# Optimization experiments

Measured on AMD Instinct MI355X. Metric: run time of the kernel, lower is better.

Reference implementation:

```python
import jax, jax.numpy as jnp
import numpy as np

B, T, C_EMBD, C_ATT = 16, 1024, 2048, 2048


def wkv(time_decay, time_first, k, v):
    """Numerically-stable RWKV WKV recurrence (matches wkv_cuda).
    time_decay/time_first: [C]; k, v: [B, T, C] -> y: [B, T, C]."""
    w = -jnp.exp(time_decay)  # [C], decay is -exp(param)
    u = time_first
    Bn, Tn, Cn = k.shape

    def step(carry, kv_t):
        aa, bb, pp = carry          # each [B, C]
        kt, vt = kv_t               # [B, C]
        ww = u + kt
        p = jnp.maximum(pp, ww)
        e1 = jnp.exp(pp - p)
        e2 = jnp.exp(ww - p)
        y = (e1 * aa + e2 * vt) / (e1 * bb + e2)
        ww2 = pp + w
        p2 = jnp.maximum(ww2, kt)
        e1b = jnp.exp(ww2 - p2)
        e2b = jnp.exp(kt - p2)
        new = (e1b * aa + e2b * vt, e1b * bb + e2b, p2)
        return new, y

    init = (jnp.zeros((Bn, Cn), k.dtype),
            jnp.zeros((Bn, Cn), k.dtype),
            jnp.full((Bn, Cn), -1e38, k.dtype))
    kT = jnp.swapaxes(k, 0, 1)  # [T, B, C]
    vT = jnp.swapaxes(v, 0, 1)
    _, ys = jax.lax.scan(step, init, (kT, vT))
    return jnp.swapaxes(ys, 0, 1)  # [B, T, C]


def setup_inputs() -> dict:
    key = jax.random.key(0)
    ks = jax.random.split(key, 10)
    xav = np.sqrt(2.0 / (C_EMBD + C_ATT))
    inp = {
        "x": jax.random.normal(ks[0], (B, T, C_EMBD), jnp.float32),
        "time_decay": jax.random.normal(ks[1], (C_ATT,), jnp.float32) * 0.02,
        "time_first": jax.random.normal(ks[2], (C_ATT,), jnp.float32) * 0.02,
        "time_mix_k": jax.random.normal(ks[3], (1, 1, C_EMBD), jnp.float32) * 0.02,
        "time_mix_v": jax.random.normal(ks[4], (1, 1, C_EMBD), jnp.float32) * 0.02,
        "time_mix_r": jax.random.normal(ks[5], (1, 1, C_EMBD), jnp.float32) * 0.02,
        "key_w": jax.random.normal(ks[6], (C_ATT, C_EMBD), jnp.float32) * xav,
        "value_w": jax.random.normal(ks[7], (C_ATT, C_EMBD), jnp.float32) * xav,
        "receptance_w": jax.random.normal(ks[8], (C_ATT, C_EMBD), jnp.float32) * xav,
        "output_w": jax.random.normal(ks[9], (C_EMBD, C_ATT), jnp.float32) * xav,
    }
    return inp


def reference(x, time_decay, time_first, time_mix_k, time_mix_v, time_mix_r,
              key_w, value_w, receptance_w, output_w):
    # time shift: xx[:, t] = x[:, t-1], xx[:, 0] = 0
    xx = jnp.pad(x, ((0, 0), (1, 0), (0, 0)))[:, :-1]
    xk = x * time_mix_k + xx * (1 - time_mix_k)
    xv = x * time_mix_v + xx * (1 - time_mix_v)
    xr = x * time_mix_r + xx * (1 - time_mix_r)
    k = jnp.einsum('btc,dc->btd', xk, key_w)
    v = jnp.einsum('btc,dc->btd', xv, value_w)
    r = jnp.einsum('btc,dc->btd', xr, receptance_w)
    sr = jax.nn.sigmoid(r)
    rwkv = sr * wkv(time_decay, time_first, k, v)
    return jnp.einsum('btd,cd->btc', rwkv, output_w)
```

## Files before the change

kernel.cpp:

```cpp
#include <hip/hip_runtime.h>
#include <hip/hip_bf16.h>

#define BB 16
#define TT 1024
#define CC 2048
#define TS 32

typedef __attribute__((ext_vector_type(4))) float f32x4;
typedef __attribute__((ext_vector_type(8))) short bf16x8;

__device__ __forceinline__ unsigned short f2bf(float f) {
  union { float f; unsigned u; } x; x.f = f;
  unsigned r = x.u + 0x7fffu + ((x.u >> 16) & 1u);
  return (unsigned short)(r >> 16);
}
__device__ __forceinline__ float bf2f(unsigned short u) {
  union { unsigned u; float f; } x; x.u = ((unsigned)u) << 16;
  return x.f;
}

__device__ __forceinline__ ushort4 mix4(float4 a, float4 b, float4 m) {
  ushort4 o;
  o.x = f2bf(a.x * m.x + b.x * (1.f - m.x));
  o.y = f2bf(a.y * m.y + b.y * (1.f - m.y));
  o.z = f2bf(a.z * m.z + b.z * (1.f - m.z));
  o.w = f2bf(a.w * m.w + b.w * (1.f - m.w));
  return o;
}

__global__ void f2bf_all(const float* __restrict__ w0, const float* __restrict__ w1,
                         const float* __restrict__ w2, const float* __restrict__ w3,
                         unsigned short* __restrict__ o0, unsigned short* __restrict__ o1,
                         unsigned short* __restrict__ o2, unsigned short* __restrict__ o3,
                         int n4each) {
  const float* ws[4] = {w0, w1, w2, w3};
  unsigned short* os[4] = {o0, o1, o2, o3};
  int total = 4 * n4each;
  for (int i = blockIdx.x * blockDim.x + threadIdx.x; i < total;
       i += gridDim.x * blockDim.x) {
    int seg = i / n4each, j = i - seg * n4each;
    float4 v = ((const float4*)ws[seg])[j];
    ushort4 o;
    o.x = f2bf(v.x); o.y = f2bf(v.y); o.z = f2bf(v.z); o.w = f2bf(v.w);
    ((ushort4*)os[seg])[j] = o;
  }
}

__global__ void mix_kernel(const float* __restrict__ x,
                           const float* __restrict__ tmk,
                           const float* __restrict__ tmv,
                           const float* __restrict__ tmr,
                           unsigned short* __restrict__ xk,
                           unsigned short* __restrict__ xv,
                           unsigned short* __restrict__ xr,
                           int t0, int Tc) {
  const int C4 = CC / 4;
  const int total = BB * Tc * C4;
  for (int g = blockIdx.x * blockDim.x + threadIdx.x; g < total;
       g += gridDim.x * blockDim.x) {
    int cg = g % C4;
    int lrow = g / C4;
    int tl = lrow % Tc;
    int b = lrow / Tc;
    int t = t0 + tl;
    size_t gidx = (size_t)(b * TT + t) * C4 + cg;
    float4 xc = ((const float4*)x)[gidx];
    float4 xp = make_float4(0.f, 0.f, 0.f, 0.f);
    if (t > 0) xp = ((const float4*)x)[gidx - C4];
    ((ushort4*)xk)[g] = mix4(xc, xp, ((const float4*)tmk)[cg]);
    ((ushort4*)xv)[g] = mix4(xc, xp, ((const float4*)tmv)[cg]);
    ((ushort4*)xr)[g] = mix4(xc, xp, ((const float4*)tmr)[cg]);
  }
}

template<bool BF16OUT>
__global__ __launch_bounds__(512, 2)
void gemm256(const unsigned short* __restrict__ A,
             const unsigned short* __restrict__ B,
             void* __restrict__ Cv, int M, int N, int K,
             int tcShift, int t0) {
  __shared__ __align__(1024) unsigned char lds[131072];
  const int tid = threadIdx.x;
  const int lane = tid & 63;
  const int wid = tid >> 6;
  const int wr = wid >> 2;
  const int wc = wid & 3;

  const int nwg = gridDim.x;
  const int cpx = nwg >> 3;
  const int bid = blockIdx.x;
  const int wg = (bid & 7) * cpx + (bid >> 3);
  const int bcolN = N >> 8;
  const int brow = wg / bcolN;
  const int bcol = wg % bcolN;

  const unsigned short* Ag = A + (size_t)(brow * 256) * K;
  const unsigned short* Bg = B + (size_t)(bcol * 256) * K;

  const int srow = tid >> 3;
  const int scolE = ((((tid & 7) * 16) ^ ((srow & 7) << 4)) >> 1);
  const int ldsWave = wid * 1024;
  const int rowB0 = ((srow >> 5) << 6) + (srow & 31);

  const int frow = lane & 15;
  const int fhi = (lane >> 4) << 4;
  const int fsw = (frow & 7) << 4;

#define STA(par, h, g, kk)                                                     \
  __builtin_amdgcn_global_load_lds(                                            \
      (const __attribute__((address_space(1))) void*)(                         \
          Ag + (size_t)(srow + (h) * 64 + (g) * 128) * K + (kk) + scolE),      \
      (__attribute__((address_space(3))) void*)(                               \
          lds + (par) * 32768 + (h) * 16384 + (g) * 8192 + ldsWave), 16, 0, 0)
#define STB(par, h, g, kk)                                                     \
  __builtin_amdgcn_global_load_lds(                                            \
      (const __attribute__((address_space(1))) void*)(                         \
          Bg + (size_t)(rowB0 + (h) * 32 + (g) * 128) * K + (kk) + scolE),     \
      (__attribute__((address_space(3))) void*)(                               \
          lds + 65536 + (par) * 32768 + (h) * 16384 + (g) * 8192 + ldsWave),   \
      16, 0, 0)

#define RD_A(par, h)                                                           \
  do { _Pragma("unroll") for (int m = 0; m < 4; ++m)                           \
       _Pragma("unroll") for (int kk = 0; kk < 2; ++kk)                        \
         af[m * 2 + kk] = *(const bf16x8*)(lds + (par) * 32768 +               \
             (h) * 16384 + (wr * 64 + m * 16 + frow) * 128 +                   \
             (((kk << 6) + fhi) ^ fsw));                                       \
  } while (0)
#define RD_B(par, h)                                                           \
  do { _Pragma("unroll") for (int n = 0; n < 2; ++n)                           \
       _Pragma("unroll") for (int kk = 0; kk < 2; ++kk)                        \
         bf[n * 2 + kk] = *(const bf16x8*)(lds + 65536 + (par) * 32768 +       \
             (h) * 16384 + (wc * 32 + n * 16 + frow) * 128 +                   \
             (((kk << 6) + fhi) ^ fsw));                                       \
  } while (0)

#define MFMA_Q(AM, AN)                                                         \
  do { __builtin_amdgcn_s_setprio(1);                                          \
       _Pragma("unroll") for (int m = 0; m < 4; ++m)                           \
       _Pragma("unroll") for (int n = 0; n < 2; ++n)                           \
       _Pragma("unroll") for (int kk = 0; kk < 2; ++kk)                        \
         acc[(AM) + m][(AN) + n] = __builtin_amdgcn_mfma_f32_16x16x32_bf16(    \
             af[m * 2 + kk], bf[n * 2 + kk], acc[(AM) + m][(AN) + n], 0, 0, 0);\
       __builtin_amdgcn_s_setprio(0); } while (0)

#define BAR __builtin_amdgcn_s_barrier()
#define VMC4 asm volatile("s_waitcnt vmcnt(4)" ::: "memory")
#define VMC0 asm volatile("s_waitcnt vmcnt(0)" ::: "memory")

  const int NI = K >> 7;

  STA(0, 0, 0, 0); STA(0, 0, 1, 0);
  STA(0, 1, 0, 0); STA(0, 1, 1, 0);
  STB(0, 0, 0, 0); STB(0, 0, 1, 0);
  STB(0, 1, 0, 0); STB(0, 1, 1, 0);
  STA(1, 0, 0, 64); STA(1, 0, 1, 64);
  STB(1, 1, 0, 64); STB(1, 1, 1, 64);
  VMC4;
  BAR;

  f32x4 acc[8][4] = {};
  bf16x8 af[8], bf[4];

  for (int i = 0; i < NI; ++i) {
    const int k1 = (2 * i + 1) << 6;
    const int k2 = (2 * i + 2) << 6;
    const int k3 = (2 * i + 3) << 6;
    const bool st = (i + 1 < NI);

    RD_A(0, 0); RD_B(0, 0);
    STB(1, 0, 0, k1); STB(1, 0, 1, k1);
    BAR; MFMA_Q(0, 0); BAR;

    RD_B(0, 1);
    STA(1, 1, 0, k1); STA(1, 1, 1, k1);
    BAR; MFMA_Q(0, 2); BAR;

    RD_A(0, 1);
    if (st) { STA(0, 0, 0, k2); STA(0, 0, 1, k2); }
    BAR; MFMA_Q(4, 2); BAR;

    RD_B(0, 0);
    if (st) { STB(0, 1, 0, k2); STB(0, 1, 1, k2); }
    BAR; MFMA_Q(4, 0);
    if (st) { VMC4; } else { VMC0; }
    BAR;

    RD_A(1, 0); RD_B(1, 0);
    if (st) { STA(0, 1, 0, k2); STA(0, 1, 1, k2); }
    BAR; MFMA_Q(0, 0); BAR;

    RD_B(1, 1);
    if (st) { STB(0, 0, 0, k2); STB(0, 0, 1, k2); }
    BAR; MFMA_Q(0, 2); BAR;

    RD_A(1, 1);
    if (st) { STA(1, 0, 0, k3); STA(1, 0, 1, k3); }
    BAR; MFMA_Q(4, 2); BAR;

    RD_B(1, 0);
    if (st) { STB(1, 1, 0, k3); STB(1, 1, 1, k3); }
    BAR; MFMA_Q(4, 0);
    if (st) { VMC4; }
    BAR;
  }
#undef STA
#undef STB
#undef RD_A
#undef RD_B
#undef MFMA_Q
#undef BAR
#undef VMC4
#undef VMC0

  const int crow0 = (lane >> 4) << 2;
  const int ccol = lane & 15;
  const int tcMask = (1 << tcShift) - 1;
#pragma unroll
  for (int am = 0; am < 8; ++am)
#pragma unroll
    for (int an = 0; an < 4; ++an) {
      const int col = bcol * 256 + wc * 64 + (an >> 1) * 32 + (an & 1) * 16 + ccol;
#pragma unroll
      for (int j = 0; j < 4; ++j) {
        int r = brow * 256 + wr * 128 + (am >> 2) * 64 + (am & 3) * 16 + crow0 + j;
        int orow = ((r >> tcShift) << 10) + t0 + (r & tcMask);
        if (BF16OUT)
          ((unsigned short*)Cv)[(size_t)orow * N + col] = f2bf(acc[am][an][j]);
        else
          ((float*)Cv)[(size_t)orow * N + col] = acc[am][an][j];
      }
    }
}

__global__ void wkv_part(const float* __restrict__ time_decay,
                         const unsigned short* __restrict__ k,
                         const unsigned short* __restrict__ v,
                         float* __restrict__ paA, float* __restrict__ paB,
                         float* __restrict__ paP, int Tc) {
  int idx = blockIdx.x * blockDim.x + threadIdx.x;
  int c = idx & (CC - 1);
  int b = (idx >> 11) & (BB - 1);
  int s = idx >> 15;
  float w = -__expf(time_decay[c]);
  float aa = 0.f, bb = 0.f, pp = -1e38f;
  size_t base = ((size_t)b * Tc + s * TS) * CC + c;
  for (int t = 0; t < TS; ++t) {
    size_t off = base + (size_t)t * CC;
    float kt = bf2f(k[off]), vt = bf2f(v[off]);
    float ww2 = pp + w;
    float p2 = fmaxf(ww2, kt);
    float e1 = __expf(ww2 - p2), e2 = __expf(kt - p2);
    aa = e1 * aa + e2 * vt;
    bb = e1 * bb + e2;
    pp = p2;
  }
  paA[idx] = aa; paB[idx] = bb; paP[idx] = pp;
}

__global__ void wkv_comb(const float* __restrict__ time_decay,
                         const float* __restrict__ paA,
                         const float* __restrict__ paB,
                         const float* __restrict__ paP,
                         float* __restrict__ inA, float* __restrict__ inB,
                         float* __restrict__ inP,
                         float* __restrict__ state, int S, int t0) {
  int idx = blockIdx.x * blockDim.x + threadIdx.x;
  int c = idx & (CC - 1);
  float w = -__expf(time_decay[c]);
  float wTs = w * (float)TS;
  float A, Bv, P;
  if (t0 == 0) { A = 0.f; Bv = 0.f; P = -1e38f; }
  else { A = state[idx]; Bv = state[32768 + idx]; P = state[65536 + idx]; }
  for (int s = 0; s < S; ++s) {
    size_t o = (size_t)s * 32768 + idx;
    inA[o] = A; inB[o] = Bv; inP[o] = P;
    float Pd = P + wTs;
    float Ps = paP[o];
    float Pn = fmaxf(Pd, Ps);
    float e1 = __expf(Pd - Pn), e2 = __expf(Ps - Pn);
    A = e1 * A + e2 * paA[o];
    Bv = e1 * Bv + e2 * paB[o];
    P = Pn;
  }
  state[idx] = A; state[32768 + idx] = Bv; state[65536 + idx] = P;
}

__global__ void wkv_out(const float* __restrict__ time_decay,
                        const float* __restrict__ time_first,
                        const unsigned short* __restrict__ k,
                        const unsigned short* __restrict__ v,
                        const unsigned short* __restrict__ r,
                        unsigned short* __restrict__ rwkv,
                        const float* __restrict__ inA,
                        const float* __restrict__ inB,
                        const float* __restrict__ inP, int Tc) {
  int idx = blockIdx.x * blockDim.x + threadIdx.x;
  int c = idx & (CC - 1);
  int b = (idx >> 11) & (BB - 1);
  int s = idx >> 15;
  float w = -__expf(time_decay[c]);
  float u = time_first[c];
  float aa = inA[idx], bb = inB[idx], pp = inP[idx];
  size_t base = ((size_t)b * Tc + s * TS) * CC + c;
  for (int t = 0; t < TS; ++t) {
    size_t off = base + (size_t)t * CC;
    float kt = bf2f(k[off]), vt = bf2f(v[off]);
    float ww = u + kt;
    float p = fmaxf(pp, ww);
    float e1 = __expf(pp - p), e2 = __expf(ww - p);
    float y = (e1 * aa + e2 * vt) / (e1 * bb + e2);
    float rr = bf2f(r[off]);
    float sr = 1.f / (1.f + __expf(-rr));
    rwkv[off] = f2bf(sr * y);
    float ww2 = pp + w;
    float p2 = fmaxf(ww2, kt);
    float e1b = __expf(ww2 - p2), e2b = __expf(kt - p2);
    aa = e1b * aa + e2b * vt;
    bb = e1b * bb + e2b;
    pp = p2;
  }
}

extern "C" void kernel_launch(void* const* d_in, const int* in_sizes, int n_in,
                              void* d_out, int out_size, void* d_ws,
                              size_t ws_size, hipStream_t stream) {
  const float* x          = (const float*)d_in[0];
  const float* time_decay = (const float*)d_in[1];
  const float* time_first = (const float*)d_in[2];
  const float* tmk        = (const float*)d_in[3];
  const float* tmv        = (const float*)d_in[4];
  const float* tmr        = (const float*)d_in[5];
  const float* key_w      = (const float*)d_in[6];
  const float* value_w    = (const float*)d_in[7];
  const float* rec_w      = (const float*)d_in[8];
  const float* out_w      = (const float*)d_in[9];
  float* out = (float*)d_out;

  const size_t WW = (size_t)CC * CC;
  const size_t wtBytes = 4 * WW * 2;
  const size_t stBytes = 3 * (size_t)BB * CC * 4;

  int Tc = 1024;
  while (Tc > 32) {
    size_t chunkBytes = (size_t)BB * Tc * CC * 12;
    if (wtBytes + stBytes + chunkBytes + 1024 <= ws_size) break;
    Tc >>= 1;
  }
  const int Mc = BB * Tc;
  const size_t NC = (size_t)Mc * CC;
  const int S = Tc / TS;

  char* p = (char*)d_ws;
  unsigned short* wk  = (unsigned short*)p; p += WW * 2;
  unsigned short* wv  = (unsigned short*)p; p += WW * 2;
  unsigned short* wrr = (unsigned short*)p; p += WW * 2;
  unsigned short* wo  = (unsigned short*)p; p += WW * 2;
  float* state        = (float*)p;          p += stBytes;
  unsigned short* kbuf= (unsigned short*)p; p += NC * 2;
  unsigned short* vbuf= (unsigned short*)p; p += NC * 2;
  unsigned short* xk  = (unsigned short*)p; p += NC * 2;
  unsigned short* xv  = (unsigned short*)p; p += NC * 2;
  unsigned short* xr  = (unsigned short*)p; p += NC * 2;
  unsigned short* rbuf= (unsigned short*)p; p += NC * 2;
  unsigned short* rwkv = xk;

  const size_t SBt = (size_t)S * 32768;
  float* paA = (float*)xv;
  float* paB = paA + SBt;
  float* paP = paB + SBt;
  float* inA = paP + SBt;
  float* inB = inA + SBt;
  float* inP = inB + SBt;

  f2bf_all<<<2048, 256, 0, stream>>>(key_w, value_w, rec_w, out_w,
                                     wk, wv, wrr, wo, (int)(WW / 4));

  int tcShift = 0;
  while ((1 << tcShift) < Tc) ++tcShift;

  const int nwg = (Mc / 256) * (CC / 256);
  int mixBlocks = (Mc * (CC / 4) + 255) / 256;
  if (mixBlocks > 4096) mixBlocks = 4096;

  for (int t0 = 0; t0 < TT; t0 += Tc) {
    mix_kernel<<<mixBlocks, 256, 0, stream>>>(x, tmk, tmv, tmr, xk, xv, xr,
                                              t0, Tc);
    gemm256<true><<<nwg, 512, 0, stream>>>(xk, wk, kbuf, Mc, CC, CC, 10, 0);
    gemm256<true><<<nwg, 512, 0, stream>>>(xv, wv, vbuf, Mc, CC, CC, 10, 0);
    wkv_part<<<S * 128, 256, 0, stream>>>(time_decay, kbuf, vbuf,
                                          paA, paB, paP, Tc);
    gemm256<true><<<nwg, 512, 0, stream>>>(xr, wrr, rbuf, Mc, CC, CC, 10, 0);
    wkv_comb<<<128, 256, 0, stream>>>(time_decay, paA, paB, paP,
                                      inA, inB, inP, state, S, t0);
    wkv_out<<<S * 128, 256, 0, stream>>>(time_decay, time_first, kbuf, vbuf,
                                         rbuf, rwkv, inA, inB, inP, Tc);
    gemm256<false><<<nwg, 512, 0, stream>>>(rwkv, wo, out, Mc, CC, CC,
                                            tcShift, t0);
  }
}
```

Measured before the change: 715.4 us.

## Fold time-mix into weights and fuse K/V/R projections into one GEMM

Precomputes bf16 weights scaled by the mix coefficients and by one minus them. The projection then becomes a single GEMM with N=6144 and K=4096, built from concatenated [x, x_shifted] inputs gathered inside the A-load address logic, using a zero buffer for t=0. This removes the separate mix kernel and its three activation buffers, and merges three GEMM launches into one. In exchange it doubles the projection FLOPs. The GEMM load schedule is also reordered with scheduling barriers and a deeper vmcnt wait.

```diff
diff --git a/kernel.cpp b/kernel.cpp
--- a/kernel.cpp
+++ b/kernel.cpp
@@ -19,66 +19,53 @@
   return x.f;
 }
 
-__device__ __forceinline__ ushort4 mix4(float4 a, float4 b, float4 m) {
-  ushort4 o;
-  o.x = f2bf(a.x * m.x + b.x * (1.f - m.x));
-  o.y = f2bf(a.y * m.y + b.y * (1.f - m.y));
-  o.z = f2bf(a.z * m.z + b.z * (1.f - m.z));
-  o.w = f2bf(a.w * m.w + b.w * (1.f - m.w));
-  return o;
-}
-
-__global__ void f2bf_all(const float* __restrict__ w0, const float* __restrict__ w1,
-                         const float* __restrict__ w2, const float* __restrict__ w3,
-                         unsigned short* __restrict__ o0, unsigned short* __restrict__ o1,
-                         unsigned short* __restrict__ o2, unsigned short* __restrict__ o3,
-                         int n4each) {
-  const float* ws[4] = {w0, w1, w2, w3};
-  unsigned short* os[4] = {o0, o1, o2, o3};
-  int total = 4 * n4each;
-  for (int i = blockIdx.x * blockDim.x + threadIdx.x; i < total;
+__global__ void f2bf_kernel(const float* __restrict__ in,
+                            unsigned short* __restrict__ out, int n4) {
+  for (int i = blockIdx.x * blockDim.x + threadIdx.x; i < n4;
        i += gridDim.x * blockDim.x) {
-    int seg = i / n4each, j = i - seg * n4each;
-    float4 v = ((const float4*)ws[seg])[j];
+    float4 v = ((const float4*)in)[i];
     ushort4 o;
     o.x = f2bf(v.x); o.y = f2bf(v.y); o.z = f2bf(v.z); o.w = f2bf(v.w);
-    ((ushort4*)os[seg])[j] = o;
-  }
-}
-
-__global__ void mix_kernel(const float* __restrict__ x,
-                           const float* __restrict__ tmk,
-                           const float* __restrict__ tmv,
-                           const float* __restrict__ tmr,
-                           unsigned short* __restrict__ xk,
-                           unsigned short* __restrict__ xv,
-                           unsigned short* __restrict__ xr,
-                           int t0, int Tc) {
-  const int C4 = CC / 4;
-  const int total = BB * Tc * C4;
+    ((ushort4*)out)[i] = o;
+  }
+}
+
+__global__ void zero_zbuf(unsigned short* __restrict__ z) {
+  z[blockIdx.x * 256 + threadIdx.x] = 0;
+}
+
+__global__ void prep_w(const float* __restrict__ w0, const float* __restrict__ w1,
+                       const float* __restrict__ w2,
+                       const float* __restrict__ m0, const float* __restrict__ m1,
+                       const float* __restrict__ m2,
+                       unsigned short* __restrict__ Wf) {
+  const int total = 6144 * 512;
   for (int g = blockIdx.x * blockDim.x + threadIdx.x; g < total;
        g += gridDim.x * blockDim.x) {
-    int cg = g % C4;
-    int lrow = g / C4;
-    int tl = lrow % Tc;
-    int b = lrow / Tc;
-    int t = t0 + tl;
-    size_t gidx = (size_t)(b * TT + t) * C4 + cg;
-    float4 xc = ((const float4*)x)[gidx];
-    float4 xp = make_float4(0.f, 0.f, 0.f, 0.f);
-    if (t > 0) xp = ((const float4*)x)[gidx - C4];
-    ((ushort4*)xk)[g] = mix4(xc, xp, ((const float4*)tmk)[cg]);
-    ((ushort4*)xv)[g] = mix4(xc, xp, ((const float4*)tmv)[cg]);
-    ((ushort4*)xr)[g] = mix4(xc, xp, ((const float4*)tmr)[cg]);
-  }
-}
-
-template<bool BF16OUT>
+    int n = g >> 9;
+    int c4 = (g & 511) << 2;
+    int which = n >> 11, nl = n & 2047;
+    const float* W  = which == 0 ? w0 : which == 1 ? w1 : w2;
+    const float* Mx = which == 0 ? m0 : which == 1 ? m1 : m2;
+    float4 wv = ((const float4*)(W + (size_t)nl * 2048))[c4 >> 2];
+    float4 mv = ((const float4*)Mx)[c4 >> 2];
+    ushort4 a, b;
+    a.x = f2bf(wv.x * mv.x); a.y = f2bf(wv.y * mv.y);
+    a.z = f2bf(wv.z * mv.z); a.w = f2bf(wv.w * mv.w);
+    b.x = f2bf(wv.x * (1.f - mv.x)); b.y = f2bf(wv.y * (1.f - mv.y));
+    b.z = f2bf(wv.z * (1.f - mv.z)); b.w = f2bf(wv.w * (1.f - mv.w));
+    ((ushort4*)(Wf + (size_t)n * 4096))[c4 >> 2] = a;
+    ((ushort4*)(Wf + (size_t)n * 4096 + 2048))[c4 >> 2] = b;
+  }
+}
+
+template<int FUSED>
 __global__ __launch_bounds__(512, 2)
-void gemm256(const unsigned short* __restrict__ A,
-             const unsigned short* __restrict__ B,
-             void* __restrict__ Cv, int M, int N, int K,
-             int tcShift, int t0) {
+void gemm8p(const unsigned short* __restrict__ A,
+            const unsigned short* __restrict__ Bw,
+            void* __restrict__ C0, void* __restrict__ C1, void* __restrict__ C2,
+            const unsigned short* __restrict__ zbuf,
+            int N, int K, int tcShift, int t0) {
   __shared__ __align__(1024) unsigned char lds[131072];
   const int tid = threadIdx.x;
   const int lane = tid & 63;
@@ -94,31 +81,43 @@
   const int brow = wg / bcolN;
   const int bcol = wg % bcolN;
 
-  const unsigned short* Ag = A + (size_t)(brow * 256) * K;
-  const unsigned short* Bg = B + (size_t)(bcol * 256) * K;
-
   const int srow = tid >> 3;
   const int scolE = ((((tid & 7) * 16) ^ ((srow & 7) << 4)) >> 1);
   const int ldsWave = wid * 1024;
   const int rowB0 = ((srow >> 5) << 6) + (srow & 31);
+  const int tcMask = (1 << tcShift) - 1;
 
   const int frow = lane & 15;
   const int fhi = (lane >> 4) << 4;
   const int fsw = (frow & 7) << 4;
 
-#define STA(par, h, g, kk)                                                     \
-  __builtin_amdgcn_global_load_lds(                                            \
-      (const __attribute__((address_space(1))) void*)(                         \
-          Ag + (size_t)(srow + (h) * 64 + (g) * 128) * K + (kk) + scolE),      \
-      (__attribute__((address_space(3))) void*)(                               \
-          lds + (par) * 32768 + (h) * 16384 + (g) * 8192 + ldsWave), 16, 0, 0)
+#define STA(par, h, g, kk) do {                                                \
+    const unsigned short* _src;                                                \
+    int _r = brow * 256 + (h) * 64 + (g) * 128 + srow;                         \
+    if (FUSED) {                                                               \
+      int _gr = ((_r >> tcShift) << 10) + t0 + (_r & tcMask);                  \
+      if ((kk) < 2048) _src = A + (size_t)_gr * 2048 + (kk) + scolE;           \
+      else {                                                                   \
+        int _t = _gr & 1023;                                                   \
+        _src = _t ? A + (size_t)(_gr - 1) * 2048 + ((kk) - 2048) + scolE       \
+                  : zbuf + ((kk) - 2048) + scolE;                              \
+      }                                                                        \
+    } else {                                                                   \
+      _src = A + (size_t)_r * K + (kk) + scolE;                                \
+    }                                                                          \
+    __builtin_amdgcn_global_load_lds(                                          \
+        (const __attribute__((address_space(1))) void*)_src,                   \
+        (__attribute__((address_space(3))) void*)(lds + (par) * 32768 +        \
+            (h) * 16384 + (g) * 8192 + ldsWave), 16, 0, 0);                    \
+  } while (0)
+
 #define STB(par, h, g, kk)                                                     \
   __builtin_amdgcn_global_load_lds(                                            \
       (const __attribute__((address_space(1))) void*)(                         \
-          Bg + (size_t)(rowB0 + (h) * 32 + (g) * 128) * K + (kk) + scolE),     \
-      (__attribute__((address_space(3))) void*)(                               \
-          lds + 65536 + (par) * 32768 + (h) * 16384 + (g) * 8192 + ldsWave),   \
-      16, 0, 0)
+          Bw + (size_t)(bcol * 256 + rowB0 + (h) * 32 + (g) * 128) * K +       \
+          (kk) + scolE),                                                       \
+      (__attribute__((address_space(3))) void*)(lds + 65536 + (par) * 32768 +  \
+          (h) * 16384 + (g) * 8192 + ldsWave), 16, 0, 0)
 
 #define RD_A(par, h)                                                           \
   do { _Pragma("unroll") for (int m = 0; m < 4; ++m)                           \
@@ -144,8 +143,9 @@
              af[m * 2 + kk], bf[n * 2 + kk], acc[(AM) + m][(AN) + n], 0, 0, 0);\
        __builtin_amdgcn_s_setprio(0); } while (0)
 
+#define SBAR __builtin_amdgcn_sched_barrier(0)
 #define BAR __builtin_amdgcn_s_barrier()
-#define VMC4 asm volatile("s_waitcnt vmcnt(4)" ::: "memory")
+#define VMC6 asm volatile("s_waitcnt vmcnt(6)" ::: "memory")
 #define VMC0 asm volatile("s_waitcnt vmcnt(0)" ::: "memory")
 
   const int NI = K >> 7;
@@ -156,52 +156,53 @@
   STB(0, 1, 0, 0); STB(0, 1, 1, 0);
   STA(1, 0, 0, 64); STA(1, 0, 1, 64);
   STB(1, 1, 0, 64); STB(1, 1, 1, 64);
-  VMC4;
+  STA(1, 1, 0, 64); STA(1, 1, 1, 64);
+  VMC6;
   BAR;
 
   f32x4 acc[8][4] = {};
   bf16x8 af[8], bf[4];
 
   for (int i = 0; i < NI; ++i) {
-    const int k1 = (2 * i + 1) << 6;
-    const int k2 = (2 * i + 2) << 6;
-    const int k3 = (2 * i + 3) << 6;
+    const int kT1 = (i << 7) + 64;
+    const int k2 = (i << 7) + 128;
+    const int k3 = (i << 7) + 192;
     const bool st = (i + 1 < NI);
 
     RD_A(0, 0); RD_B(0, 0);
-    STB(1, 0, 0, k1); STB(1, 0, 1, k1);
-    BAR; MFMA_Q(0, 0); BAR;
+    STB(1, 0, 0, kT1); STB(1, 0, 1, kT1);
+    SBAR; BAR; MFMA_Q(0, 0); BAR;
 
     RD_B(0, 1);
-    STA(1, 1, 0, k1); STA(1, 1, 1, k1);
-    BAR; MFMA_Q(0, 2); BAR;
+    if (st) { STA(0, 0, 0, k2); STA(0, 0, 1, k2); }
+    SBAR; BAR; MFMA_Q(0, 2); BAR;
 
     RD_A(0, 1);
-    if (st) { STA(0, 0, 0, k2); STA(0, 0, 1, k2); }
-    BAR; MFMA_Q(4, 2); BAR;
+    if (st) { STB(0, 1, 0, k2); STB(0, 1, 1, k2); }
+    SBAR; BAR; MFMA_Q(4, 2); BAR;
 
     RD_B(0, 0);
-    if (st) { STB(0, 1, 0, k2); STB(0, 1, 1, k2); }
-    BAR; MFMA_Q(4, 0);
-    if (st) { VMC4; } else { VMC0; }
+    if (st) { STA(0, 1, 0, k2); STA(0, 1, 1, k2); }
+    SBAR; BAR; MFMA_Q(4, 0);
+    if (st) { VMC6; } else { VMC0; }
     BAR;
 
     RD_A(1, 0); RD_B(1, 0);
-    if (st) { STA(0, 1, 0, k2); STA(0, 1, 1, k2); }
-    BAR; MFMA_Q(0, 0); BAR;
+    if (st) { STB(0, 0, 0, k2); STB(0, 0, 1, k2); }
+    SBAR; BAR; MFMA_Q(0, 0); BAR;
 
     RD_B(1, 1);
-    if (st) { STB(0, 0, 0, k2); STB(0, 0, 1, k2); }
-    BAR; MFMA_Q(0, 2); BAR;
+    if (st) { STA(1, 0, 0, k3); STA(1, 0, 1, k3); }
+    SBAR; BAR; MFMA_Q(0, 2); BAR;
 
     RD_A(1, 1);
-    if (st) { STA(1, 0, 0, k3); STA(1, 0, 1, k3); }
-    BAR; MFMA_Q(4, 2); BAR;
+    if (st) { STB(1, 1, 0, k3); STB(1, 1, 1, k3); }
+    SBAR; BAR; MFMA_Q(4, 2); BAR;
 
     RD_B(1, 0);
-    if (st) { STB(1, 1, 0, k3); STB(1, 1, 1, k3); }
-    BAR; MFMA_Q(4, 0);
-    if (st) { VMC4; }
+    if (st) { STA(1, 1, 0, k3); STA(1, 1, 1, k3); }
+    SBAR; BAR; MFMA_Q(4, 0);
+    if (st) { VMC6; }
     BAR;
   }
 #undef STA
@@ -209,28 +210,48 @@
 #undef RD_A
 #undef RD_B
 #undef MFMA_Q
+#undef SBAR
 #undef BAR
-#undef VMC4
+#undef VMC6
 #undef VMC0
 
   const int crow0 = (lane >> 4) << 2;
   const int ccol = lane & 15;
-  const int tcMask = (1 << tcShift) - 1;
-#pragma unroll
-  for (int am = 0; am < 8; ++am)
-#pragma unroll
-    for (int an = 0; an < 4; ++an) {
-      const int col = bcol * 256 + wc * 64 + (an >> 1) * 32 + (an & 1) * 16 + ccol;
-#pragma unroll
-      for (int j = 0; j < 4; ++j) {
-        int r = brow * 256 + wr * 128 + (am >> 2) * 64 + (am & 3) * 16 + crow0 + j;
-        int orow = ((r >> tcShift) << 10) + t0 + (r & tcMask);
-        if (BF16OUT)
-          ((unsigned short*)Cv)[(size_t)orow * N + col] = f2bf(acc[am][an][j]);
-        else
-          ((float*)Cv)[(size_t)orow * N + col] = acc[am][an][j];
+  if (FUSED) {
+    const int which = bcol >> 3;
+    unsigned short* outp = which == 0 ? (unsigned short*)C0
+                         : which == 1 ? (unsigned short*)C1
+                                      : (unsigned short*)C2;
+    const int colb = (bcol & 7) * 256 + wc * 64;
+#pragma unroll
+    for (int am = 0; am < 8; ++am)
+#pragma unroll
+      for (int an = 0; an < 4; ++an) {
+        const int col = colb + (an >> 1) * 32 + (an & 1) * 16 + ccol;
+#pragma unroll
+        for (int j = 0; j < 4; ++j) {
+          int r = brow * 256 + wr * 128 + (am >> 2) * 64 + (am & 3) * 16 +
+                  crow0 + j;
+          outp[(size_t)r * 2048 + col] = f2bf(acc[am][an][j]);
+        }
       }
-    }
+  } else {
+    float* outp = (float*)C0;
+#pragma unroll
+    for (int am = 0; am < 8; ++am)
+#pragma unroll
+      for (int an = 0; an < 4; ++an) {
+        const int col = bcol * 256 + wc * 64 + (an >> 1) * 32 + (an & 1) * 16 +
+                        ccol;
+#pragma unroll
+        for (int j = 0; j < 4; ++j) {
+          int r = brow * 256 + wr * 128 + (am >> 2) * 64 + (am & 3) * 16 +
+                  crow0 + j;
+          int orow = ((r >> tcShift) << 10) + t0 + (r & tcMask);
+          outp[(size_t)orow * N + col] = acc[am][an][j];
+        }
+      }
+  }
 }
 
 __global__ void wkv_part(const float* __restrict__ time_decay,
@@ -337,14 +358,19 @@
   const float* out_w      = (const float*)d_in[9];
   float* out = (float*)d_out;
 
-  const size_t WW = (size_t)CC * CC;
-  const size_t wtBytes = 4 * WW * 2;
-  const size_t stBytes = 3 * (size_t)BB * CC * 4;
+  const int MM = BB * TT;
+  const size_t xbfBytes = (size_t)MM * CC * 2;
+  const size_t WfBytes  = (size_t)6144 * 4096 * 2;
+  const size_t woBytes  = (size_t)CC * CC * 2;
+  const size_t zBytes   = 4096 * 2;
+  const size_t stBytes  = 3 * (size_t)BB * CC * 4;
+  const size_t fixed = xbfBytes + WfBytes + woBytes + zBytes + stBytes;
 
   int Tc = 1024;
   while (Tc > 32) {
-    size_t chunkBytes = (size_t)BB * Tc * CC * 12;
-    if (wtBytes + stBytes + chunkBytes + 1024 <= ws_size) break;
+    size_t chunkBytes = (size_t)BB * Tc * CC * 8 +
+                        (size_t)(Tc / TS) * 6 * 32768 * 4;
+    if (fixed + chunkBytes + 1024 <= ws_size) break;
     Tc >>= 1;
   }
   const int Mc = BB * Tc;
@@ -352,50 +378,43 @@
   const int S = Tc / TS;
 
   char* p = (char*)d_ws;
-  unsigned short* wk  = (unsigned short*)p; p += WW * 2;
-  unsigned short* wv  = (unsigned short*)p; p += WW * 2;
-  unsigned short* wrr = (unsigned short*)p; p += WW * 2;
-  unsigned short* wo  = (unsigned short*)p; p += WW * 2;
+  unsigned short* xbf = (unsigned short*)p; p += xbfBytes;
+  unsigned short* Wf  = (unsigned short*)p; p += WfBytes;
+  unsigned short* wobf= (unsigned short*)p; p += woBytes;
+  unsigned short* zbuf= (unsigned short*)p; p += zBytes;
   float* state        = (float*)p;          p += stBytes;
   unsigned short* kbuf= (unsigned short*)p; p += NC * 2;
   unsigned short* vbuf= (unsigned short*)p; p += NC * 2;
-  unsigned short* xk  = (unsigned short*)p; p += NC * 2;
-  unsigned short* xv  = (unsigned short*)p; p += NC * 2;
-  unsigned short* xr  = (unsigned short*)p; p += NC * 2;
   unsigned short* rbuf= (unsigned short*)p; p += NC * 2;
-  unsigned short* rwkv = xk;
-
-  const size_t SBt = (size_t)S * 32768;
-  float* paA = (float*)xv;
-  float* paB = paA + SBt;
-  float* paP = paB + SBt;
-  float* inA = paP + SBt;
-  float* inB = inA + SBt;
-  float* inP = inB + SBt;
-
-  f2bf_all<<<2048, 256, 0, stream>>>(key_w, value_w, rec_w, out_w,
-                                     wk, wv, wrr, wo, (int)(WW / 4));
+  unsigned short* rwkv= (unsigned short*)p; p += NC * 2;
+  float* paA = (float*)p;
+  float* paB = paA + (size_t)S * 32768;
+  float* paP = paB + (size_t)S * 32768;
+  float* inA = paP + (size_t)S * 32768;
+  float* inB = inA + (size_t)S * 32768;
+  float* inP = inB + (size_t)S * 32768;
+
+  zero_zbuf<<<16, 256, 0, stream>>>(zbuf);
+  f2bf_kernel<<<2048, 256, 0, stream>>>(x, xbf, MM * CC / 4);
+  prep_w<<<2048, 256, 0, stream>>>(key_w, value_w, rec_w, tmk, tmv, tmr, Wf);
+  f2bf_kernel<<<1024, 256, 0, stream>>>(out_w, wobf, CC * CC / 4);
 
   int tcShift = 0;
   while ((1 << tcShift) < Tc) ++tcShift;
 
-  const int nwg = (Mc / 256) * (CC / 256);
-  int mixBlocks = (Mc * (CC / 4) + 255) / 256;
-  if (mixBlocks > 4096) mixBlocks = 4096;
+  const int nwgF = (Mc / 256) * (6144 / 256);
+  const int nwgO = (Mc / 256) * (CC / 256);
 
   for (int t0 = 0; t0 < TT; t0 += Tc) {
-    mix_kernel<<<mixBlocks, 256, 0, stream>>>(x, tmk, tmv, tmr, xk, xv, xr,
-                                              t0, Tc);
-    gemm256<true><<<nwg, 512, 0, stream>>>(xk, wk, kbuf, Mc, CC, CC, 10, 0);
-    gemm256<true><<<nwg, 512, 0, stream>>>(xv, wv, vbuf, Mc, CC, CC, 10, 0);
+    gemm8p<1><<<nwgF, 512, 0, stream>>>(xbf, Wf, kbuf, vbuf, rbuf, zbuf,
+                                        6144, 4096, tcShift, t0);
     wkv_part<<<S * 128, 256, 0, stream>>>(time_decay, kbuf, vbuf,
                                           paA, paB, paP, Tc);
-    gemm256<true><<<nwg, 512, 0, stream>>>(xr, wrr, rbuf, Mc, CC, CC, 10, 0);
     wkv_comb<<<128, 256, 0, stream>>>(time_decay, paA, paB, paP,
                                       inA, inB, inP, state, S, t0);
     wkv_out<<<S * 128, 256, 0, stream>>>(time_decay, time_first, kbuf, vbuf,
                                          rbuf, rwkv, inA, inB, inP, Tc);
-    gemm256<false><<<nwg, 512, 0, stream>>>(rwkv, wo, out, Mc, CC, CC,
-                                            tcShift, t0);
-  }
-}
+    gemm8p<0><<<nwgO, 512, 0, stream>>>(rwkv, wobf, out, nullptr, nullptr,
+                                        zbuf, CC, CC, tcShift, t0);
+  }
+}
```

Result: slower. 1.041 ms (+45.5%).

## Load GEMM B operand directly from global into registers, stage only A in LDS

Applied to the files above, without the earlier changes.

Rewrites the 256x256 bf16 GEMM so that only the A tile is staged through LDS via global_load_lds, while each wave loads its B fragments straight from global memory into registers, double-buffered across K tiles. LDS use drops from 128KB to 64KB, and the fine-grained multi-barrier schedule becomes a simpler two-stage ping-pong with one barrier per 64-wide K tile. The aim is to cut LDS traffic and barrier overhead. The cost is uncoalesced, more register-hungry B loads, with no LDS reuse of B across the two wave rows.

```diff
diff --git a/kernel.cpp b/kernel.cpp
--- a/kernel.cpp
+++ b/kernel.cpp
@@ -75,11 +75,10 @@
 
 template<bool BF16OUT>
 __global__ __launch_bounds__(512, 2)
-void gemm256(const unsigned short* __restrict__ A,
-             const unsigned short* __restrict__ B,
-             void* __restrict__ Cv, int M, int N, int K,
-             int tcShift, int t0) {
-  __shared__ __align__(1024) unsigned char lds[131072];
+void gemm_bd(const unsigned short* __restrict__ A,
+             const unsigned short* __restrict__ Bw,
+             void* __restrict__ Cv, int N, int K, int tcShift, int t0) {
+  __shared__ __align__(1024) unsigned char lds[65536];
   const int tid = threadIdx.x;
   const int lane = tid & 63;
   const int wid = tid >> 6;
@@ -94,124 +93,75 @@
   const int brow = wg / bcolN;
   const int bcol = wg % bcolN;
 
-  const unsigned short* Ag = A + (size_t)(brow * 256) * K;
-  const unsigned short* Bg = B + (size_t)(bcol * 256) * K;
-
   const int srow = tid >> 3;
   const int scolE = ((((tid & 7) * 16) ^ ((srow & 7) << 4)) >> 1);
-  const int ldsWave = wid * 1024;
-  const int rowB0 = ((srow >> 5) << 6) + (srow & 31);
-
   const int frow = lane & 15;
-  const int fhi = (lane >> 4) << 4;
+  const int fk16 = (lane >> 4) << 4;
   const int fsw = (frow & 7) << 4;
 
-#define STA(par, h, g, kk)                                                     \
-  __builtin_amdgcn_global_load_lds(                                            \
-      (const __attribute__((address_space(1))) void*)(                         \
-          Ag + (size_t)(srow + (h) * 64 + (g) * 128) * K + (kk) + scolE),      \
-      (__attribute__((address_space(3))) void*)(                               \
-          lds + (par) * 32768 + (h) * 16384 + (g) * 8192 + ldsWave), 16, 0, 0)
-#define STB(par, h, g, kk)                                                     \
-  __builtin_amdgcn_global_load_lds(                                            \
-      (const __attribute__((address_space(1))) void*)(                         \
-          Bg + (size_t)(rowB0 + (h) * 32 + (g) * 128) * K + (kk) + scolE),     \
-      (__attribute__((address_space(3))) void*)(                               \
-          lds + 65536 + (par) * 32768 + (h) * 16384 + (g) * 8192 + ldsWave),   \
-      16, 0, 0)
-
-#define RD_A(par, h)                                                           \
-  do { _Pragma("unroll") for (int m = 0; m < 4; ++m)                           \
-       _Pragma("unroll") for (int kk = 0; kk < 2; ++kk)                        \
-         af[m * 2 + kk] = *(const bf16x8*)(lds + (par) * 32768 +               \
-             (h) * 16384 + (wr * 64 + m * 16 + frow) * 128 +                   \
-             (((kk << 6) + fhi) ^ fsw));                                       \
+  const unsigned short* Arow = A + (size_t)(brow * 256 + srow) * K + scolE;
+  const unsigned short* Bb =
+      Bw + (size_t)(bcol * 256 + wc * 64 + frow) * K + ((lane >> 4) << 3);
+
+  f32x4 acc[8][4] = {};
+  bf16x8 bA[8], bB[8], af[4];
+
+#define STAGEA(bufOff, tk) do {                                                \
+    _Pragma("unroll") for (int g = 0; g < 4; ++g)                              \
+      __builtin_amdgcn_global_load_lds(                                        \
+          (const __attribute__((address_space(1))) void*)(                     \
+              Arow + (size_t)(g * 64) * K + (tk)),                             \
+          (__attribute__((address_space(3))) void*)(                           \
+              lds + (bufOff) + g * 8192 + tid * 16), 16, 0, 0);                \
   } while (0)
-#define RD_B(par, h)                                                           \
-  do { _Pragma("unroll") for (int n = 0; n < 2; ++n)                           \
-       _Pragma("unroll") for (int kk = 0; kk < 2; ++kk)                        \
-         bf[n * 2 + kk] = *(const bf16x8*)(lds + 65536 + (par) * 32768 +       \
-             (h) * 16384 + (wc * 32 + n * 16 + frow) * 128 +                   \
-             (((kk << 6) + fhi) ^ fsw));                                       \
+
+#define BLOAD(dst, tk) do {                                                    \
+    _Pragma("unroll") for (int n = 0; n < 4; ++n)                              \
+    _Pragma("unroll") for (int kk = 0; kk < 2; ++kk)                           \
+      dst[n * 2 + kk] =                                                        \
+          *(const bf16x8*)(Bb + (size_t)(n * 16) * K + (tk) + kk * 32);        \
   } while (0)
 
-#define MFMA_Q(AM, AN)                                                         \
-  do { __builtin_amdgcn_s_setprio(1);                                          \
-       _Pragma("unroll") for (int m = 0; m < 4; ++m)                           \
-       _Pragma("unroll") for (int n = 0; n < 2; ++n)                           \
-       _Pragma("unroll") for (int kk = 0; kk < 2; ++kk)                        \
-         acc[(AM) + m][(AN) + n] = __builtin_amdgcn_mfma_f32_16x16x32_bf16(    \
-             af[m * 2 + kk], bf[n * 2 + kk], acc[(AM) + m][(AN) + n], 0, 0, 0);\
-       __builtin_amdgcn_s_setprio(0); } while (0)
-
-#define BAR __builtin_amdgcn_s_barrier()
-#define VMC4 asm volatile("s_waitcnt vmcnt(4)" ::: "memory")
-#define VMC0 asm volatile("s_waitcnt vmcnt(0)" ::: "memory")
-
-  const int NI = K >> 7;
-
-  STA(0, 0, 0, 0); STA(0, 0, 1, 0);
-  STA(0, 1, 0, 0); STA(0, 1, 1, 0);
-  STB(0, 0, 0, 0); STB(0, 0, 1, 0);
-  STB(0, 1, 0, 0); STB(0, 1, 1, 0);
-  STA(1, 0, 0, 64); STA(1, 0, 1, 64);
-  STB(1, 1, 0, 64); STB(1, 1, 1, 64);
-  VMC4;
-  BAR;
-
-  f32x4 acc[8][4] = {};
-  bf16x8 af[8], bf[4];
-
-  for (int i = 0; i < NI; ++i) {
-    const int k1 = (2 * i + 1) << 6;
-    const int k2 = (2 * i + 2) << 6;
-    const int k3 = (2 * i + 3) << 6;
-    const bool st = (i + 1 < NI);
-
-    RD_A(0, 0); RD_B(0, 0);
-    STB(1, 0, 0, k1); STB(1, 0, 1, k1);
-    BAR; MFMA_Q(0, 0); BAR;
-
-    RD_B(0, 1);
-    STA(1, 1, 0, k1); STA(1, 1, 1, k1);
-    BAR; MFMA_Q(0, 2); BAR;
-
-    RD_A(0, 1);
-    if (st) { STA(0, 0, 0, k2); STA(0, 0, 1, k2); }
-    BAR; MFMA_Q(4, 2); BAR;
-
-    RD_B(0, 0);
-    if (st) { STB(0, 1, 0, k2); STB(0, 1, 1, k2); }
-    BAR; MFMA_Q(4, 0);
-    if (st) { VMC4; } else { VMC0; }
-    BAR;
-
-    RD_A(1, 0); RD_B(1, 0);
-    if (st) { STA(0, 1, 0, k2); STA(0, 1, 1, k2); }
-    BAR; MFMA_Q(0, 0); BAR;
-
-    RD_B(1, 1);
-    if (st) { STB(0, 0, 0, k2); STB(0, 0, 1, k2); }
-    BAR; MFMA_Q(0, 2); BAR;
-
-    RD_A(1, 1);
-    if (st) { STA(1, 0, 0, k3); STA(1, 0, 1, k3); }
-    BAR; MFMA_Q(4, 2); BAR;
-
-    RD_B(1, 0);
-    if (st) { STB(1, 1, 0, k3); STB(1, 1, 1, k3); }
-    BAR; MFMA_Q(4, 0);
-    if (st) { VMC4; }
-    BAR;
-  }
-#undef STA
-#undef STB
-#undef RD_A
-#undef RD_B
-#undef MFMA_Q
-#undef BAR
-#undef VMC4
-#undef VMC0
+#define COMPUTE(bufOff, bfr) do {                                              \
+    _Pragma("unroll") for (int mq = 0; mq < 4; ++mq) {                         \
+      _Pragma("unroll") for (int mi = 0; mi < 2; ++mi)                         \
+      _Pragma("unroll") for (int kk = 0; kk < 2; ++kk) {                       \
+        const int row = wr * 128 + (mq * 2 + mi) * 16 + frow;                  \
+        af[mi * 2 + kk] = *(const bf16x8*)(lds + (bufOff) + row * 128 +        \
+                            (((kk << 6) + fk16) ^ fsw));                       \
+      }                                                                        \
+      __builtin_amdgcn_s_setprio(1);                                           \
+      _Pragma("unroll") for (int mi = 0; mi < 2; ++mi)                         \
+      _Pragma("unroll") for (int n = 0; n < 4; ++n)                            \
+      _Pragma("unroll") for (int kk = 0; kk < 2; ++kk)                         \
+        acc[mq * 2 + mi][n] = __builtin_amdgcn_mfma_f32_16x16x32_bf16(         \
+            af[mi * 2 + kk], bfr[n * 2 + kk], acc[mq * 2 + mi][n], 0, 0, 0);   \
+      __builtin_amdgcn_s_setprio(0);                                           \
+    } } while (0)
+
+#define TILE_TOP do {                                                          \
+    asm volatile("s_waitcnt vmcnt(8)" ::: "memory");                           \
+    __builtin_amdgcn_sched_barrier(0);                                         \
+    __builtin_amdgcn_s_barrier();                                              \
+  } while (0)
+
+  const int NT = K >> 6;
+
+  STAGEA(0, 0);
+  BLOAD(bA, 0);
+
+  for (int t = 0; t < NT; t += 2) {
+    TILE_TOP;
+    if (t + 1 < NT) { STAGEA(32768, (t + 1) * 64); BLOAD(bB, (t + 1) * 64); }
+    COMPUTE(0, bA);
+    TILE_TOP;
+    if (t + 2 < NT) { STAGEA(0, (t + 2) * 64); BLOAD(bA, (t + 2) * 64); }
+    COMPUTE(32768, bB);
+  }
+#undef STAGEA
+#undef BLOAD
+#undef COMPUTE
+#undef TILE_TOP
 
   const int crow0 = (lane >> 4) << 2;
   const int ccol = lane & 15;
@@ -220,10 +170,10 @@
   for (int am = 0; am < 8; ++am)
 #pragma unroll
     for (int an = 0; an < 4; ++an) {
-      const int col = bcol * 256 + wc * 64 + (an >> 1) * 32 + (an & 1) * 16 + ccol;
+      const int col = bcol * 256 + wc * 64 + an * 16 + ccol;
 #pragma unroll
       for (int j = 0; j < 4; ++j) {
-        int r = brow * 256 + wr * 128 + (am >> 2) * 64 + (am & 3) * 16 + crow0 + j;
+        int r = brow * 256 + wr * 128 + am * 16 + crow0 + j;
         int orow = ((r >> tcShift) << 10) + t0 + (r & tcMask);
         if (BF16OUT)
           ((unsigned short*)Cv)[(size_t)orow * N + col] = f2bf(acc[am][an][j]);
@@ -386,16 +336,16 @@
   for (int t0 = 0; t0 < TT; t0 += Tc) {
     mix_kernel<<<mixBlocks, 256, 0, stream>>>(x, tmk, tmv, tmr, xk, xv, xr,
                                               t0, Tc);
-    gemm256<true><<<nwg, 512, 0, stream>>>(xk, wk, kbuf, Mc, CC, CC, 10, 0);
-    gemm256<true><<<nwg, 512, 0, stream>>>(xv, wv, vbuf, Mc, CC, CC, 10, 0);
+    gemm_bd<true><<<nwg, 512, 0, stream>>>(xk, wk, kbuf, CC, CC, 10, 0);
+    gemm_bd<true><<<nwg, 512, 0, stream>>>(xv, wv, vbuf, CC, CC, 10, 0);
     wkv_part<<<S * 128, 256, 0, stream>>>(time_decay, kbuf, vbuf,
                                           paA, paB, paP, Tc);
-    gemm256<true><<<nwg, 512, 0, stream>>>(xr, wrr, rbuf, Mc, CC, CC, 10, 0);
+    gemm_bd<true><<<nwg, 512, 0, stream>>>(xr, wrr, rbuf, CC, CC, 10, 0);
     wkv_comb<<<128, 256, 0, stream>>>(time_decay, paA, paB, paP,
                                       inA, inB, inP, state, S, t0);
     wkv_out<<<S * 128, 256, 0, stream>>>(time_decay, time_first, kbuf, vbuf,
                                          rbuf, rwkv, inA, inB, inP, Tc);
-    gemm256<false><<<nwg, 512, 0, stream>>>(rwkv, wo, out, Mc, CC, CC,
+    gemm_bd<false><<<nwg, 512, 0, stream>>>(rwkv, wo, out, CC, CC,
                                             tcShift, t0);
   }
 }
```

After: 983.6 us. 1.37x slower.

## Keep both B half-tiles in registers and reorder GEMM LDS prefetch schedule

Applied to the files above, without the earlier changes.

The GEMM main loop now holds both B k-halves in registers (bf grows from 4 to 8 fragments), so the redundant RD_B reload before the fourth MFMA quarter is gone. The global-to-LDS stores are reshuffled so the A tile for the next half is issued earlier, and the vmcnt wait goes from 4 to 6 outstanding loads. Explicit lgkmcnt(0) waits and sched_barriers are added around each MFMA block to pin the instruction ordering. The larger register footprint may pressure occupancy at 2 blocks of 512 threads, and the stricter scheduling barriers could limit compiler interleaving.

```diff
diff --git a/kernel.cpp b/kernel.cpp
--- a/kernel.cpp
+++ b/kernel.cpp
@@ -77,8 +77,7 @@
 __global__ __launch_bounds__(512, 2)
 void gemm256(const unsigned short* __restrict__ A,
              const unsigned short* __restrict__ B,
-             void* __restrict__ Cv, int M, int N, int K,
-             int tcShift, int t0) {
+             void* __restrict__ Cv, int N, int K, int tcShift, int t0) {
   __shared__ __align__(1024) unsigned char lds[131072];
   const int tid = threadIdx.x;
   const int lane = tid & 63;
@@ -116,9 +115,8 @@
   __builtin_amdgcn_global_load_lds(                                            \
       (const __attribute__((address_space(1))) void*)(                         \
           Bg + (size_t)(rowB0 + (h) * 32 + (g) * 128) * K + (kk) + scolE),     \
-      (__attribute__((address_space(3))) void*)(                               \
-          lds + 65536 + (par) * 32768 + (h) * 16384 + (g) * 8192 + ldsWave),   \
-      16, 0, 0)
+      (__attribute__((address_space(3))) void*)(lds + 65536 + (par) * 32768 +  \
+          (h) * 16384 + (g) * 8192 + ldsWave), 16, 0, 0)
 
 #define RD_A(par, h)                                                           \
   do { _Pragma("unroll") for (int m = 0; m < 4; ++m)                           \
@@ -130,22 +128,26 @@
 #define RD_B(par, h)                                                           \
   do { _Pragma("unroll") for (int n = 0; n < 2; ++n)                           \
        _Pragma("unroll") for (int kk = 0; kk < 2; ++kk)                        \
-         bf[n * 2 + kk] = *(const bf16x8*)(lds + 65536 + (par) * 32768 +       \
-             (h) * 16384 + (wc * 32 + n * 16 + frow) * 128 +                   \
+         bf[(h) * 4 + n * 2 + kk] = *(const bf16x8*)(lds + 65536 +             \
+             (par) * 32768 + (h) * 16384 + (wc * 32 + n * 16 + frow) * 128 +   \
              (((kk << 6) + fhi) ^ fsw));                                       \
   } while (0)
 
-#define MFMA_Q(AM, AN)                                                         \
+#define MFMA_Q(AM, AN, HB)                                                     \
   do { __builtin_amdgcn_s_setprio(1);                                          \
        _Pragma("unroll") for (int m = 0; m < 4; ++m)                           \
        _Pragma("unroll") for (int n = 0; n < 2; ++n)                           \
        _Pragma("unroll") for (int kk = 0; kk < 2; ++kk)                        \
          acc[(AM) + m][(AN) + n] = __builtin_amdgcn_mfma_f32_16x16x32_bf16(    \
-             af[m * 2 + kk], bf[n * 2 + kk], acc[(AM) + m][(AN) + n], 0, 0, 0);\
+             af[m * 2 + kk], bf[(HB) + n * 2 + kk], acc[(AM) + m][(AN) + n],   \
+             0, 0, 0);                                                         \
        __builtin_amdgcn_s_setprio(0); } while (0)
 
+#define SBAR __builtin_amdgcn_sched_barrier(0)
 #define BAR __builtin_amdgcn_s_barrier()
-#define VMC4 asm volatile("s_waitcnt vmcnt(4)" ::: "memory")
+#define LGKM0 do { asm volatile("s_waitcnt lgkmcnt(0)" ::: "memory");          \
+                   __builtin_amdgcn_sched_barrier(0); } while (0)
+#define VMC6 asm volatile("s_waitcnt vmcnt(6)" ::: "memory")
 #define VMC0 asm volatile("s_waitcnt vmcnt(0)" ::: "memory")
 
   const int NI = K >> 7;
@@ -156,52 +158,51 @@
   STB(0, 1, 0, 0); STB(0, 1, 1, 0);
   STA(1, 0, 0, 64); STA(1, 0, 1, 64);
   STB(1, 1, 0, 64); STB(1, 1, 1, 64);
-  VMC4;
+  STA(1, 1, 0, 64); STA(1, 1, 1, 64);
+  VMC6;
   BAR;
 
   f32x4 acc[8][4] = {};
-  bf16x8 af[8], bf[4];
+  bf16x8 af[8], bf[8];
 
   for (int i = 0; i < NI; ++i) {
-    const int k1 = (2 * i + 1) << 6;
-    const int k2 = (2 * i + 2) << 6;
-    const int k3 = (2 * i + 3) << 6;
+    const int kT1 = (i << 7) + 64;
+    const int k2 = (i << 7) + 128;
+    const int k3 = (i << 7) + 192;
     const bool st = (i + 1 < NI);
 
     RD_A(0, 0); RD_B(0, 0);
-    STB(1, 0, 0, k1); STB(1, 0, 1, k1);
-    BAR; MFMA_Q(0, 0); BAR;
+    STB(1, 0, 0, kT1); STB(1, 0, 1, kT1);
+    SBAR; BAR; LGKM0; MFMA_Q(0, 0, 0); BAR;
 
     RD_B(0, 1);
-    STA(1, 1, 0, k1); STA(1, 1, 1, k1);
-    BAR; MFMA_Q(0, 2); BAR;
+    if (st) { STA(0, 0, 0, k2); STA(0, 0, 1, k2); }
+    SBAR; BAR; LGKM0; MFMA_Q(0, 2, 4); BAR;
 
     RD_A(0, 1);
-    if (st) { STA(0, 0, 0, k2); STA(0, 0, 1, k2); }
-    BAR; MFMA_Q(4, 2); BAR;
-
-    RD_B(0, 0);
     if (st) { STB(0, 1, 0, k2); STB(0, 1, 1, k2); }
-    BAR; MFMA_Q(4, 0);
-    if (st) { VMC4; } else { VMC0; }
+    SBAR; BAR; LGKM0; MFMA_Q(4, 2, 4); BAR;
+
+    if (st) { STA(0, 1, 0, k2); STA(0, 1, 1, k2); }
+    SBAR; BAR; LGKM0; MFMA_Q(4, 0, 0);
+    if (st) { VMC6; } else { VMC0; }
     BAR;
 
     RD_A(1, 0); RD_B(1, 0);
-    if (st) { STA(0, 1, 0, k2); STA(0, 1, 1, k2); }
-    BAR; MFMA_Q(0, 0); BAR;
+    if (st) { STB(0, 0, 0, k2); STB(0, 0, 1, k2); }
+    SBAR; BAR; LGKM0; MFMA_Q(0, 0, 0); BAR;
 
     RD_B(1, 1);
-    if (st) { STB(0, 0, 0, k2); STB(0, 0, 1, k2); }
-    BAR; MFMA_Q(0, 2); BAR;
+    if (st) { STA(1, 0, 0, k3); STA(1, 0, 1, k3); }
+    SBAR; BAR; LGKM0; MFMA_Q(0, 2, 4); BAR;
 
     RD_A(1, 1);
-    if (st) { STA(1, 0, 0, k3); STA(1, 0, 1, k3); }
-    BAR; MFMA_Q(4, 2); BAR;
-
-    RD_B(1, 0);
     if (st) { STB(1, 1, 0, k3); STB(1, 1, 1, k3); }
-    BAR; MFMA_Q(4, 0);
-    if (st) { VMC4; }
+    SBAR; BAR; LGKM0; MFMA_Q(4, 2, 4); BAR;
+
+    if (st) { STA(1, 1, 0, k3); STA(1, 1, 1, k3); }
+    SBAR; BAR; LGKM0; MFMA_Q(4, 0, 0);
+    if (st) { VMC6; }
     BAR;
   }
 #undef STA
@@ -209,8 +210,10 @@
 #undef RD_A
 #undef RD_B
 #undef MFMA_Q
+#undef SBAR
 #undef BAR
-#undef VMC4
+#undef LGKM0
+#undef VMC6
 #undef VMC0
 
   const int crow0 = (lane >> 4) << 2;
@@ -386,16 +389,16 @@
   for (int t0 = 0; t0 < TT; t0 += Tc) {
     mix_kernel<<<mixBlocks, 256, 0, stream>>>(x, tmk, tmv, tmr, xk, xv, xr,
                                               t0, Tc);
-    gemm256<true><<<nwg, 512, 0, stream>>>(xk, wk, kbuf, Mc, CC, CC, 10, 0);
-    gemm256<true><<<nwg, 512, 0, stream>>>(xv, wv, vbuf, Mc, CC, CC, 10, 0);
+    gemm256<true><<<nwg, 512, 0, stream>>>(xk, wk, kbuf, CC, CC, 10, 0);
+    gemm256<true><<<nwg, 512, 0, stream>>>(xv, wv, vbuf, CC, CC, 10, 0);
     wkv_part<<<S * 128, 256, 0, stream>>>(time_decay, kbuf, vbuf,
                                           paA, paB, paP, Tc);
-    gemm256<true><<<nwg, 512, 0, stream>>>(xr, wrr, rbuf, Mc, CC, CC, 10, 0);
+    gemm256<true><<<nwg, 512, 0, stream>>>(xr, wrr, rbuf, CC, CC, 10, 0);
     wkv_comb<<<128, 256, 0, stream>>>(time_decay, paA, paB, paP,
                                       inA, inB, inP, state, S, t0);
     wkv_out<<<S * 128, 256, 0, stream>>>(time_decay, time_first, kbuf, vbuf,
                                          rbuf, rwkv, inA, inB, inP, Tc);
-    gemm256<false><<<nwg, 512, 0, stream>>>(rwkv, wo, out, Mc, CC, CC,
+    gemm256<false><<<nwg, 512, 0, stream>>>(rwkv, wo, out, CC, CC,
                                             tcShift, t0);
   }
 }
```

After: 714.1 us. Within noise of the previous version (-0.2%).
